# Kernel tuning notes

Measured on AMD Instinct MI355X. Metric: run time of the kernel, lower is better.

## Reference

```python
import jax, jax.numpy as jnp
import numpy as np

FH, FW = 38, 50          # stride-16 feature map of a 608x800 image
N_ROIS = 512
SCALE = 1.0 / 16.0
R = 7                    # roi_size -> 7x7 position-sensitive bins, 2x2 crop per bin
OUT_DIM = 10


def _conv(x, w, b, pad):
    # NCHW conv, stride 1, asymmetric 'same' padding for (k,1)/(1,k) kernels
    y = jax.lax.conv_general_dilated(
        x, w, (1, 1), [(pad[0], pad[0]), (pad[1], pad[1])],
        dimension_numbers=('NCHW', 'OIHW', 'NCHW'))
    return y + b[None, :, None, None]


def setup_inputs() -> dict:
    key = jax.random.key(0)
    ks = jax.random.split(key, 20)
    x = jax.random.normal(ks[0], (1, 2048, FH, FW), jnp.float32)
    # rois: unnormalized [x1,y1,x2,y2] in image coordinates, strictly inside the image
    img_h, img_w = FH * 16.0, FW * 16.0
    u = jax.random.uniform(ks[1], (N_ROIS, 4))
    x1 = u[:, 0] * (img_w * 0.5)
    y1 = u[:, 1] * (img_h * 0.5)
    x2 = x1 + 16.0 + u[:, 2] * (img_w - 17.0 - x1)
    y2 = y1 + 16.0 + u[:, 3] * (img_h - 17.0 - y1)
    rois = jnp.stack([x1, y1, x2, y2], axis=1)
    std = 0.01  # normal_init(0, 0.01)
    p = lambda k, shape: jax.random.normal(k, shape, jnp.float32) * std
    inp = {
        'x': x, 'rois': rois,
        'w_col_max': p(ks[2], (256, 2048, 15, 1)), 'b_col_max': jnp.zeros((256,), jnp.float32),
        'w_col':     p(ks[3], (490, 256, 1, 15)),  'b_col':     jnp.zeros((490,), jnp.float32),
        'w_row_max': p(ks[4], (256, 2048, 1, 15)), 'b_row_max': jnp.zeros((256,), jnp.float32),
        'w_row':     p(ks[5], (490, 256, 15, 1)),  'b_row':     jnp.zeros((490,), jnp.float32),
        'w_fc1':   p(ks[6], (2048, 490)), 'b_fc1':   jnp.zeros((2048,), jnp.float32),
        'w_score': p(ks[7], (81, 2048)),  'b_score': jnp.zeros((81,), jnp.float32),
        'w_loc':   p(ks[8], (324, 2048)), 'b_loc':   jnp.zeros((324,), jnp.float32),
    }
    return inp


def reference(x, rois, w_col_max, b_col_max, w_col, b_col,
              w_row_max, b_row_max, w_row, b_row,
              w_fc1, b_fc1, w_score, b_score, w_loc, b_loc):
    # ---- GlobalContextModule: large separable 15-tap convs ----
    h_col = _conv(_conv(x, w_col_max, b_col_max, (7, 0)), w_col, b_col, (0, 7))
    h_row = _conv(_conv(x, w_row_max, b_row_max, (0, 7)), w_row, b_row, (7, 0))
    h = jax.nn.relu(h_col + h_row)  # [1, 490, H, W]
    H, W = h.shape[2], h.shape[3]

    # ---- position-sensitive crop-and-resize + per-bin max, fully vectorized ----
    b = rois * SCALE / jnp.array([W, H, W, H], jnp.float32)  # normalized [x1,y1,x2,y2]
    xmin, ymin, xmax, ymax = b[:, 0], b[:, 1], b[:, 2], b[:, 3]
    step_x = (xmax - xmin) / R
    step_y = (ymax - ymin) / R
    # sample offsets: bin index (0..R-1) + crop sample (0 or 1); crop size 2 => samples at bin edges
    g = jnp.arange(R, dtype=jnp.float32)[None, :, None] + jnp.arange(2, dtype=jnp.float32)[None, None, :]
    ys = (ymin[:, None, None] + g * step_y[:, None, None]) * (H - 1)  # [N, R, 2]
    xs = (xmin[:, None, None] + g * step_x[:, None, None]) * (W - 1)  # [N, R, 2]

    def idx_w(v, vmax):
        v0 = jnp.floor(v)
        f = v - v0
        i0 = jnp.clip(v0, 0, vmax - 1).astype(jnp.int32)
        i1 = jnp.clip(v0 + 1.0, 0, vmax - 1).astype(jnp.int32)
        return i0, i1, f

    yi0, yi1, wy = idx_w(ys, H)
    xi0, xi1, wx = idx_w(xs, W)

    feat = h[0].reshape(R * R, OUT_DIM, H, W).transpose(0, 2, 3, 1)  # [49, H, W, 10]
    bidx = (jnp.arange(R)[:, None] * R + jnp.arange(R)[None, :])[None, :, :, None, None]  # [1,R,R,1,1]
    Y0 = yi0[:, :, None, :, None]; Y1 = yi1[:, :, None, :, None]  # [N,R,1,2,1]
    X0 = xi0[:, None, :, None, :]; X1 = xi1[:, None, :, None, :]  # [N,1,R,1,2]
    WY = wy[:, :, None, :, None, None]
    WX = wx[:, None, :, None, :, None]

    v00 = feat[bidx, Y0, X0]; v01 = feat[bidx, Y0, X1]
    v10 = feat[bidx, Y1, X0]; v11 = feat[bidx, Y1, X1]  # [N,R,R,2,2,10]
    top = v00 + (v01 - v00) * WX
    bot = v10 + (v11 - v10) * WX
    val = top + (bot - top) * WY
    pooled = val.max(axis=(3, 4))                       # [N, R, R, 10]
    flat = pooled.reshape(pooled.shape[0], -1)          # [N, 490], order = bin*10 + c

    fc1 = jax.nn.relu(flat @ w_fc1.T + b_fc1)           # [N, 2048]
    roi_cls_locs = fc1 @ w_loc.T + b_loc                # [N, 324]
    roi_scores = fc1 @ w_score.T + b_score              # [N, 81]
    return roi_cls_locs, roi_scores
```

## Files before the change

kernel.cpp:

```cpp
#include <hip/hip_runtime.h>
#include <math.h>

#define FW 50
#define FH 38
#define NPIX 1900
#define NROIS 512

#define CSH 2470
#define CSV 2650

typedef __bf16 bf16x8 __attribute__((ext_vector_type(8)));
typedef float  f32x4  __attribute__((ext_vector_type(4)));

__device__ __forceinline__ unsigned short f2b(float f) {
    unsigned int u = __float_as_uint(f);
    unsigned int r = (u + 0x7fffu + ((u >> 16) & 1u)) >> 16;
    return (unsigned short)r;
}


__global__ __launch_bounds__(256) void zero_us(unsigned short* __restrict__ p, int n) {
    int i = (blockIdx.x * 256 + threadIdx.x) * 8;
    if (i < n) { uint4 z; z.x = z.y = z.z = z.w = 0u; *(uint4*)(p + i) = z; }
}

__global__ __launch_bounds__(256) void cvt_bf16(
    const float* __restrict__ in, unsigned short* __restrict__ out, int n)
{
    int i = (blockIdx.x * 256 + threadIdx.x) * 4;
    if (i >= n) return;
    float4 v = *(const float4*)(in + i);
    ushort2 a, b;
    a.x = f2b(v.x); a.y = f2b(v.y);
    b.x = f2b(v.z); b.y = f2b(v.w);
    *(ushort2*)(out + i)     = a;
    *(ushort2*)(out + i + 2) = b;
}

__global__ __launch_bounds__(256) void cvt_pad(
    const float* __restrict__ in, unsigned short* __restrict__ out,
    int rows, int Kin, int Kout)
{
    int idx = blockIdx.x * 256 + threadIdx.x;
    if (idx >= rows * Kout) return;
    int rw = idx / Kout, k = idx - rw * Kout;
    out[idx] = (k < Kin) ? f2b(in[(size_t)rw * Kin + k]) : (unsigned short)0;
}

__global__ __launch_bounds__(256) void repack_w(
    const float* __restrict__ w, unsigned short* __restrict__ out, int n)
{
    int idx = blockIdx.x * 256 + threadIdx.x;
    if (idx >= n) return;
    int t = idx & 15;
    int oc = idx >> 4;
    out[idx] = (t < 15) ? f2b(w[oc * 15 + t]) : (unsigned short)0;
}

__global__ __launch_bounds__(256) void xpad_h(
    const float* __restrict__ xs, unsigned short* __restrict__ out)
{
    int idx = blockIdx.x * 256 + threadIdx.x;
    if (idx >= 2048 * CSH) return;
    int c = idx / CSH;
    int rem = idx - c * CSH;
    int y = rem / 65;
    int xc = rem - y * 65 - 7;
    unsigned short v = 0;
    if (xc >= 0 && xc < FW) v = f2b(xs[(c * FH + y) * FW + xc]);
    out[idx] = v;
}

__global__ __launch_bounds__(256) void xpad_v(
    const float* __restrict__ xs, unsigned short* __restrict__ out)
{
    int idx = blockIdx.x * 256 + threadIdx.x;
    if (idx >= 2048 * CSV) return;
    int c = idx / CSV;
    int rem = idx - c * CSV;
    int xx = rem / 53;
    int yc = rem - xx * 53 - 7;
    unsigned short v = 0;
    if (yc >= 0 && yc < FH) v = f2b(xs[(c * FH + yc) * FW + xx]);
    out[idx] = v;
}

__global__ __launch_bounds__(256) void conv_tap(
    const unsigned short* __restrict__ Wt,
    const unsigned short* __restrict__ Xp,
    float* __restrict__ P,
    int M, int Kp, int Mpad, int CS, int yMul, int xMul,
    int zMask, int zBits, int yMask, int xShift)
{
    const int id = blockIdx.x;
    const int zt = id & zMask;
    const int yt = (id >> zBits) & yMask;
    const int xt = id >> xShift;
    const int nsplit = zMask + 1;

    const int Ks = Kp / nsplit;
    const int k0 = zt * Ks;
    const int tid  = threadIdx.x;
    const int lane = tid & 63;
    const int wave = tid >> 6;
    const int mbase = yt * 128;
    const int pbase = xt * 64;

    __shared__ unsigned short As[128][40];
    __shared__ unsigned short Bt[64][40];

    const int a_row = tid >> 1;
    const int a_k16 = (tid & 1) << 4;
    const int a_src = min(mbase + a_row, M - 1);
    const unsigned short* Abase = Wt + (size_t)a_src * Kp + a_k16;

    const int b_pix = tid >> 2;
    const int q     = tid & 3;
    int p = pbase + b_pix;
    if (p > NPIX - 1) p = NPIX - 1;
    const int py = p / FW, px = p - py * FW;
    const int pixBase = py * yMul + px * xMul;
    const int eoff = pixBase + ((q & 1) << 3);
    const unsigned* __restrict__ Bdw = (const unsigned*)Xp;

    f32x4 acc[4][2];
#pragma unroll
    for (int i = 0; i < 4; ++i)
#pragma unroll
        for (int j = 0; j < 2; ++j)
#pragma unroll
            for (int r = 0; r < 4; ++r) acc[i][j][r] = 0.f;

    const int wy = (wave >> 1) * 64;
    const int wx = (wave & 1) * 32;
    const int lm = lane & 15;
    const int l8 = (lane >> 4) * 8;

    uint4 aR0, aR1;
    unsigned d[5];

    auto loadA = [&](int kt) {
        aR0 = *(const uint4*)(Abase + kt);
        aR1 = *(const uint4*)(Abase + kt + 8);
    };
    auto loadB = [&](int kt) {
        const int cg = (kt >> 4) + (q >> 1);
        const unsigned base = ((unsigned)(cg * CS + eoff)) >> 1;
#pragma unroll
        for (int j = 0; j < 5; ++j) d[j] = Bdw[base + j];
    };

    loadA(k0); loadB(k0);
    const unsigned sh = ((unsigned)(pixBase & 1)) << 4;

    for (int kt = k0; kt < k0 + Ks; kt += 32) {
        unsigned ob[4];
#pragma unroll
        for (int j = 0; j < 4; ++j)
            ob[j] = __builtin_amdgcn_alignbit(d[j + 1], d[j], sh);
        *(uint4*)&As[a_row][a_k16]     = aR0;
        *(uint4*)&As[a_row][a_k16 + 8] = aR1;
        *(uint4*)&Bt[b_pix][q << 3] = *(uint4*)&ob[0];
        __syncthreads();

        if (kt + 32 < k0 + Ks) { loadA(kt + 32); loadB(kt + 32); }

        bf16x8 af[4], bfr[2];
#pragma unroll
        for (int i = 0; i < 4; ++i)
            af[i]  = __builtin_bit_cast(bf16x8, *(const uint4*)&As[wy + i * 16 + lm][l8]);
#pragma unroll
        for (int j = 0; j < 2; ++j)
            bfr[j] = __builtin_bit_cast(bf16x8, *(const uint4*)&Bt[wx + j * 16 + lm][l8]);

#pragma unroll
        for (int i = 0; i < 4; ++i)
#pragma unroll
            for (int j = 0; j < 2; ++j)
                acc[i][j] = __builtin_amdgcn_mfma_f32_16x16x32_bf16(af[i], bfr[j], acc[i][j], 0, 0, 0);
        __syncthreads();
    }

    float* Pp = P + (size_t)zt * Mpad * NPIX;
#pragma unroll
    for (int i = 0; i < 4; ++i) {
        const int m0 = mbase + wy + i * 16 + (lane >> 4) * 4;
#pragma unroll
        for (int j = 0; j < 2; ++j) {
            const int pp = pbase + wx + j * 16 + lm;
            if (pp < NPIX) {
#pragma unroll
                for (int r = 0; r < 4; ++r)
                    Pp[(size_t)(m0 + r) * NPIX + pp] = acc[i][j][r];
            }
        }
    }
}

__global__ void reduce_pad(
    const float* __restrict__ P, int Mpad, int nsplit,
    const float* __restrict__ bias, int M,
    unsigned short* __restrict__ outb, int CS, int yMul, int xMul)
{
    int idx = blockIdx.x * 256 + threadIdx.x;
    if (idx >= M * NPIX) return;
    int o = idx / NPIX;
    int p = idx - o * NPIX;
    float s = bias[o];
    for (int sp = 0; sp < nsplit; ++sp)
        s += P[((size_t)sp * Mpad + o) * NPIX + p];
    int y = p / FW, x = p - y * FW;
    outb[(size_t)o * CS + y * yMul + x * xMul + 7] = f2b(s);
}

__global__ void reduce_bias(
    const float* __restrict__ P, int Mpad, int nsplit,
    const float* __restrict__ bias, int M,
    const float* __restrict__ addbuf, int relu,
    float* __restrict__ outf)
{
    int idx = blockIdx.x * blockDim.x + threadIdx.x;
    if (idx >= M * NPIX) return;
    int o = idx / NPIX;
    int p = idx - o * NPIX;
    float s = bias[o];
    for (int sp = 0; sp < nsplit; ++sp)
        s += P[((size_t)sp * Mpad + o) * NPIX + p];
    if (addbuf) s += addbuf[idx];
    if (relu) s = fmaxf(s, 0.f);
    outf[idx] = s;
}

__global__ __launch_bounds__(512) void pool_kernel(
    const float* __restrict__ h, const float* __restrict__ rois,
    unsigned short* __restrict__ pooledb)
{
    int n = blockIdx.x;
    int k = threadIdx.x;
    if (k >= 490) {
        pooledb[(size_t)n * 512 + k] = 0;
        return;
    }
    float x1 = rois[n * 4 + 0], y1 = rois[n * 4 + 1];
    float x2 = rois[n * 4 + 2], y2 = rois[n * 4 + 3];
    float xmin = x1 * (1.f / 16.f) / 50.f;
    float ymin = y1 * (1.f / 16.f) / 38.f;
    float xmax = x2 * (1.f / 16.f) / 50.f;
    float ymax = y2 * (1.f / 16.f) / 38.f;
    float step_x = (xmax - xmin) / 7.f;
    float step_y = (ymax - ymin) / 7.f;
    int bin = k / 10;
    int bi = bin / 7, bj = bin - bi * 7;
    const float* ch = h + (size_t)k * NPIX;
    float m = -INFINITY;
#pragma unroll
    for (int sy = 0; sy < 2; ++sy) {
        float yv = (ymin + (float)(bi + sy) * step_y) * 37.f;
        float y0 = floorf(yv);
        float fy = yv - y0;
        int yi0 = min(max((int)y0, 0), 37);
        int yi1 = min(max((int)y0 + 1, 0), 37);
#pragma unroll
        for (int sx = 0; sx < 2; ++sx) {
            float xv = (xmin + (float)(bj + sx) * step_x) * 49.f;
            float x0 = floorf(xv);
            float fx = xv - x0;
            int xi0 = min(max((int)x0, 0), 49);
            int xi1 = min(max((int)x0 + 1, 0), 49);
            float v00 = ch[yi0 * FW + xi0], v01 = ch[yi0 * FW + xi1];
            float v10 = ch[yi1 * FW + xi0], v11 = ch[yi1 * FW + xi1];
            float top = v00 + (v01 - v00) * fx;
            float bot = v10 + (v11 - v10) * fx;
            float val = top + (bot - top) * fy;
            m = fmaxf(m, val);
        }
    }
    pooledb[(size_t)n * 512 + k] = f2b(m);
}

__global__ __launch_bounds__(256) void fc_mfma(
    const unsigned short* __restrict__ Wb,
    const unsigned short* __restrict__ Act,
    float* __restrict__ P, int M, int Kld, int Mpad)
{
    const int Ks = Kld / gridDim.z;
    const int k0 = blockIdx.z * Ks;
    const int tid  = threadIdx.x;
    const int lane = tid & 63;
    const int wave = tid >> 6;
    const int mbase = blockIdx.x * 64;
    const int nbase = blockIdx.y * 64;

    __shared__ unsigned short As[64][40];
    __shared__ unsigned short Bs[64][40];

    const int s_r  = tid >> 2;
    const int s_k8 = (tid & 3) << 3;
    const int a_row = mbase + s_r;
    const bool a_ok = a_row < M;
    const unsigned short* Abase = Wb + (size_t)a_row * Kld + s_k8;
    const unsigned short* Bbase = Act + (size_t)(nbase + s_r) * Kld + s_k8;

    f32x4 acc[2][2];
#pragma unroll
    for (int i = 0; i < 2; ++i)
#pragma unroll
        for (int j = 0; j < 2; ++j)
#pragma unroll
            for (int r = 0; r < 4; ++r) acc[i][j][r] = 0.f;

    const int mh = (wave >> 1) * 32;
    const int nh = (wave & 1) * 32;
    const int lm = lane & 15;
    const int l8 = (lane >> 4) * 8;

    uint4 aReg, bReg;
    if (a_ok) aReg = *(const uint4*)(Abase + k0);
    else { aReg.x = aReg.y = aReg.z = aReg.w = 0u; }
    bReg = *(const uint4*)(Bbase + k0);

    for (int kt = k0; kt < k0 + Ks; kt += 32) {
        *(uint4*)&As[s_r][s_k8] = aReg;
        *(uint4*)&Bs[s_r][s_k8] = bReg;
        __syncthreads();

        if (kt + 32 < k0 + Ks) {
            if (a_ok) aReg = *(const uint4*)(Abase + kt + 32);
            bReg = *(const uint4*)(Bbase + kt + 32);
        }

        bf16x8 a0 = __builtin_bit_cast(bf16x8, *(const uint4*)&As[mh + lm][l8]);
        bf16x8 a1 = __builtin_bit_cast(bf16x8, *(const uint4*)&As[mh + 16 + lm][l8]);
        bf16x8 b0 = __builtin_bit_cast(bf16x8, *(const uint4*)&Bs[nh + lm][l8]);
        bf16x8 b1 = __builtin_bit_cast(bf16x8, *(const uint4*)&Bs[nh + 16 + lm][l8]);

        acc[0][0] = __builtin_amdgcn_mfma_f32_16x16x32_bf16(a0, b0, acc[0][0], 0, 0, 0);
        acc[0][1] = __builtin_amdgcn_mfma_f32_16x16x32_bf16(a0, b1, acc[0][1], 0, 0, 0);
        acc[1][0] = __builtin_amdgcn_mfma_f32_16x16x32_bf16(a1, b0, acc[1][0], 0, 0, 0);
        acc[1][1] = __builtin_amdgcn_mfma_f32_16x16x32_bf16(a1, b1, acc[1][1], 0, 0, 0);
        __syncthreads();
    }

#pragma unroll
    for (int ms = 0; ms < 2; ++ms)
#pragma unroll
        for (int ns = 0; ns < 2; ++ns) {
            int n  = nbase + nh + ns * 16 + lm;
            int m0 = mbase + mh + ms * 16 + (lane >> 4) * 4;
            float* Pp = P + ((size_t)blockIdx.z * NROIS + n) * Mpad + m0;
            *(f32x4*)Pp = acc[ms][ns];
        }
}

__global__ void fc_reduce(
    const float* __restrict__ P, int Mpad, int M, int nsplit,
    const float* __restrict__ bias, int relu,
    float* __restrict__ outf, unsigned short* __restrict__ outb)
{
    int idx = blockIdx.x * 256 + threadIdx.x;
    if (idx >= NROIS * M) return;
    int n = idx / M, m = idx - n * M;
    float s = bias[m];
    for (int sp = 0; sp < nsplit; ++sp)
        s += P[((size_t)sp * NROIS + n) * Mpad + m];
    if (relu) s = fmaxf(s, 0.f);
    if (outf) outf[idx] = s;
    if (outb) outb[idx] = f2b(s);
}

extern "C" void kernel_launch(void* const* d_in, const int* in_sizes, int n_in,
                              void* d_out, int out_size, void* d_ws, size_t ws_size,
                              hipStream_t stream) {
    const float* x         = (const float*)d_in[0];
    const float* rois      = (const float*)d_in[1];
    const float* w_col_max = (const float*)d_in[2];
    const float* b_col_max = (const float*)d_in[3];
    const float* w_col     = (const float*)d_in[4];
    const float* b_col     = (const float*)d_in[5];
    const float* w_row_max = (const float*)d_in[6];
    const float* b_row_max = (const float*)d_in[7];
    const float* w_row     = (const float*)d_in[8];
    const float* b_row     = (const float*)d_in[9];
    const float* w_fc1     = (const float*)d_in[10];
    const float* b_fc1     = (const float*)d_in[11];
    const float* w_score   = (const float*)d_in[12];
    const float* b_score   = (const float*)d_in[13];
    const float* w_loc     = (const float*)d_in[14];
    const float* b_loc     = (const float*)d_in[15];

    float* part = (float*)d_ws;
    unsigned short* XvU   = (unsigned short*)(part + 7782400);
    unsigned short* XhU   = XvU + 5427264;
    unsigned short* wbig  = XhU + 5058624;
    unsigned short* wc16  = wbig + 8388608;
    unsigned short* wr16  = wc16 + 2007040;
    unsigned short* c1colb= wr16 + 2007040;
    unsigned short* c1rowb= c1colb + 632384;
    unsigned short* wfc1b = c1rowb + 678464;
    unsigned short* pooledb = wfc1b + 1048576;
    unsigned short* fc1b  = pooledb + 262144;
    unsigned short* wlocb = fc1b + 1048576;
    unsigned short* wscoreb = wlocb + 663552;
    float* hcol = (float*)XvU;
    float* h    = (float*)XhU;

    xpad_v<<<21200, 256, 0, stream>>>(x, XvU);
    xpad_h<<<19760, 256, 0, stream>>>(x, XhU);
    zero_us<<<309, 256, 0, stream>>>(c1colb, 632384);
    zero_us<<<332, 256, 0, stream>>>(c1rowb, 678464);
    repack_w<<<32768, 256, 0, stream>>>(w_col_max, wbig, 8388608);
    repack_w<<<7840, 256, 0, stream>>>(w_col, wc16, 2007040);
    repack_w<<<7840, 256, 0, stream>>>(w_row, wr16, 2007040);
    cvt_pad <<<4096, 256, 0, stream>>>(w_fc1, wfc1b, 2048, 490, 512);
    cvt_bf16<<<648,  256, 0, stream>>>(w_loc, wlocb, 663552);
    cvt_bf16<<<162,  256, 0, stream>>>(w_score, wscoreb, 165888);

    conv_tap<<<960, 256, 0, stream>>>(wbig, XvU, part, 256, 32768, 256, CSV, 1, 53, 15, 4, 1, 5);
    reduce_pad<<<1900, 256, 0, stream>>>(part, 256, 16, b_col_max, 256, c1colb, CSH, 65, 1);
    repack_w<<<32768, 256, 0, stream>>>(w_row_max, wbig, 8388608);
    conv_tap<<<960, 256, 0, stream>>>(wbig, XhU, part, 256, 32768, 256, CSH, 65, 1, 15, 4, 1, 5);
    reduce_pad<<<1900, 256, 0, stream>>>(part, 256, 16, b_row_max, 256, c1rowb, CSV, 1, 53);

    conv_tap<<<960, 256, 0, stream>>>(wc16, c1colb, part, 490, 4096, 512, CSH, 65, 1, 7, 3, 3, 5);
    reduce_bias<<<3637, 256, 0, stream>>>(part, 512, 8, b_col, 490, nullptr, 0, hcol);
    conv_tap<<<960, 256, 0, stream>>>(wr16, c1rowb, part, 490, 4096, 512, CSV, 1, 53, 7, 3, 3, 5);
    reduce_bias<<<3637, 256, 0, stream>>>(part, 512, 8, b_row, 490, hcol, 1, h);

    pool_kernel<<<512, 512, 0, stream>>>(h, rois, pooledb);

    float* out = (float*)d_out;
    fc_mfma<<<dim3(32, 8, 2), 256, 0, stream>>>(wfc1b, pooledb, part, 2048, 512, 2048);
    fc_reduce<<<4096, 256, 0, stream>>>(part, 2048, 2048, 2, b_fc1, 1, nullptr, fc1b);
    fc_mfma<<<dim3(6, 8, 4), 256, 0, stream>>>(wlocb, fc1b, part, 324, 2048, 384);
    fc_reduce<<<648, 256, 0, stream>>>(part, 384, 324, 4, b_loc, 0, out, nullptr);
    fc_mfma<<<dim3(2, 8, 8), 256, 0, stream>>>(wscoreb, fc1b, part, 81, 2048, 128);
    fc_reduce<<<162, 256, 0, stream>>>(part, 128, 81, 8, b_score, 0, out + 512 * 324, nullptr);
}
```

Measured before the change: 465.0 us.

## Enlarge conv GEMM tile to 128x128 with 32x32 MFMA and double-buffered LDS

The conv_tap GEMM now uses a 128-pixel tile instead of 64, with each wave computing a 64x64 sub-tile through 32x32x16 bf16 MFMAs, which halves the launched blocks. LDS is double-buffered, so the trailing barrier per k-step is removed and each iteration keeps a single sync. Each B-load thread now fetches 9 dwords, covering 16 channels per pixel. The aim is more reuse of A and B per LDS load and less synchronisation, at the cost of fewer blocks (480) for occupancy and more registers per thread. The two zeroing launches are merged into one.

```diff
diff --git a/kernel.cpp b/kernel.cpp
--- a/kernel.cpp
+++ b/kernel.cpp
@@ -11,6 +11,7 @@
 
 typedef __bf16 bf16x8 __attribute__((ext_vector_type(8)));
 typedef float  f32x4  __attribute__((ext_vector_type(4)));
+typedef float  f32x16 __attribute__((ext_vector_type(16)));
 
 __device__ __forceinline__ unsigned short f2b(float f) {
     unsigned int u = __float_as_uint(f);
@@ -104,94 +105,102 @@
     const int lane = tid & 63;
     const int wave = tid >> 6;
     const int mbase = yt * 128;
-    const int pbase = xt * 64;
-
-    __shared__ unsigned short As[128][40];
-    __shared__ unsigned short Bt[64][40];
+    const int pbase = xt * 128;
+
+    __shared__ unsigned short As[2][128][40];
+    __shared__ unsigned short Bt[2][128][40];
 
     const int a_row = tid >> 1;
     const int a_k16 = (tid & 1) << 4;
     const int a_src = min(mbase + a_row, M - 1);
     const unsigned short* Abase = Wt + (size_t)a_src * Kp + a_k16;
 
-    const int b_pix = tid >> 2;
-    const int q     = tid & 3;
+    const int b_pix = tid >> 1;
+    const int bh    = tid & 1;
     int p = pbase + b_pix;
     if (p > NPIX - 1) p = NPIX - 1;
     const int py = p / FW, px = p - py * FW;
     const int pixBase = py * yMul + px * xMul;
-    const int eoff = pixBase + ((q & 1) << 3);
     const unsigned* __restrict__ Bdw = (const unsigned*)Xp;
 
-    f32x4 acc[4][2];
-#pragma unroll
-    for (int i = 0; i < 4; ++i)
+    f32x16 acc[2][2];
+#pragma unroll
+    for (int i = 0; i < 2; ++i)
 #pragma unroll
         for (int j = 0; j < 2; ++j)
 #pragma unroll
-            for (int r = 0; r < 4; ++r) acc[i][j][r] = 0.f;
+            for (int r = 0; r < 16; ++r) acc[i][j][r] = 0.f;
 
     const int wy = (wave >> 1) * 64;
-    const int wx = (wave & 1) * 32;
-    const int lm = lane & 15;
-    const int l8 = (lane >> 4) * 8;
+    const int wx = (wave & 1) * 64;
+    const int l5 = lane & 31;
+    const int l8 = (lane >> 5) * 8;
 
     uint4 aR0, aR1;
-    unsigned d[5];
+    unsigned d[9];
 
     auto loadA = [&](int kt) {
         aR0 = *(const uint4*)(Abase + kt);
         aR1 = *(const uint4*)(Abase + kt + 8);
     };
     auto loadB = [&](int kt) {
-        const int cg = (kt >> 4) + (q >> 1);
-        const unsigned base = ((unsigned)(cg * CS + eoff)) >> 1;
-#pragma unroll
-        for (int j = 0; j < 5; ++j) d[j] = Bdw[base + j];
+        const int cg = (kt >> 4) + bh;
+        const unsigned base = ((unsigned)(cg * CS + pixBase)) >> 1;
+#pragma unroll
+        for (int j = 0; j < 9; ++j) d[j] = Bdw[base + j];
     };
 
     loadA(k0); loadB(k0);
     const unsigned sh = ((unsigned)(pixBase & 1)) << 4;
 
+    int buf = 0;
     for (int kt = k0; kt < k0 + Ks; kt += 32) {
-        unsigned ob[4];
-#pragma unroll
-        for (int j = 0; j < 4; ++j)
+        unsigned ob[8];
+#pragma unroll
+        for (int j = 0; j < 8; ++j)
             ob[j] = __builtin_amdgcn_alignbit(d[j + 1], d[j], sh);
-        *(uint4*)&As[a_row][a_k16]     = aR0;
-        *(uint4*)&As[a_row][a_k16 + 8] = aR1;
-        *(uint4*)&Bt[b_pix][q << 3] = *(uint4*)&ob[0];
+        *(uint4*)&As[buf][a_row][a_k16]     = aR0;
+        *(uint4*)&As[buf][a_row][a_k16 + 8] = aR1;
+        *(uint4*)&Bt[buf][b_pix][bh * 16]     = *(uint4*)&ob[0];
+        *(uint4*)&Bt[buf][b_pix][bh * 16 + 8] = *(uint4*)&ob[4];
         __syncthreads();
 
         if (kt + 32 < k0 + Ks) { loadA(kt + 32); loadB(kt + 32); }
 
-        bf16x8 af[4], bfr[2];
-#pragma unroll
-        for (int i = 0; i < 4; ++i)
-            af[i]  = __builtin_bit_cast(bf16x8, *(const uint4*)&As[wy + i * 16 + lm][l8]);
-#pragma unroll
-        for (int j = 0; j < 2; ++j)
-            bfr[j] = __builtin_bit_cast(bf16x8, *(const uint4*)&Bt[wx + j * 16 + lm][l8]);
-
-#pragma unroll
-        for (int i = 0; i < 4; ++i)
-#pragma unroll
-            for (int j = 0; j < 2; ++j)
-                acc[i][j] = __builtin_amdgcn_mfma_f32_16x16x32_bf16(af[i], bfr[j], acc[i][j], 0, 0, 0);
-        __syncthreads();
+        bf16x8 af[2][2], bfr[2][2];
+#pragma unroll
+        for (int i = 0; i < 2; ++i)
+#pragma unroll
+            for (int kk = 0; kk < 2; ++kk) {
+                af[i][kk]  = __builtin_bit_cast(bf16x8,
+                    *(const uint4*)&As[buf][wy + i * 32 + l5][kk * 16 + l8]);
+                bfr[i][kk] = __builtin_bit_cast(bf16x8,
+                    *(const uint4*)&Bt[buf][wx + i * 32 + l5][kk * 16 + l8]);
+            }
+#pragma unroll
+        for (int kk = 0; kk < 2; ++kk)
+#pragma unroll
+            for (int i = 0; i < 2; ++i)
+#pragma unroll
+                for (int j = 0; j < 2; ++j)
+                    acc[i][j] = __builtin_amdgcn_mfma_f32_32x32x16_bf16(
+                        af[i][kk], bfr[j][kk], acc[i][j], 0, 0, 0);
+        buf ^= 1;
     }
 
     float* Pp = P + (size_t)zt * Mpad * NPIX;
 #pragma unroll
-    for (int i = 0; i < 4; ++i) {
-        const int m0 = mbase + wy + i * 16 + (lane >> 4) * 4;
+    for (int i = 0; i < 2; ++i) {
+        const int mb = mbase + wy + i * 32 + (lane >> 5) * 4;
 #pragma unroll
         for (int j = 0; j < 2; ++j) {
-            const int pp = pbase + wx + j * 16 + lm;
+            const int pp = pbase + wx + j * 32 + l5;
             if (pp < NPIX) {
 #pragma unroll
-                for (int r = 0; r < 4; ++r)
-                    Pp[(size_t)(m0 + r) * NPIX + pp] = acc[i][j][r];
+                for (int r = 0; r < 16; ++r) {
+                    const int m = mb + (r & 3) + 8 * (r >> 2);
+                    Pp[(size_t)m * NPIX + pp] = acc[i][j][r];
+                }
             }
         }
     }
@@ -406,8 +415,7 @@
 
     xpad_v<<<21200, 256, 0, stream>>>(x, XvU);
     xpad_h<<<19760, 256, 0, stream>>>(x, XhU);
-    zero_us<<<309, 256, 0, stream>>>(c1colb, 632384);
-    zero_us<<<332, 256, 0, stream>>>(c1rowb, 678464);
+    zero_us<<<641, 256, 0, stream>>>(c1colb, 1310848);
     repack_w<<<32768, 256, 0, stream>>>(w_col_max, wbig, 8388608);
     repack_w<<<7840, 256, 0, stream>>>(w_col, wc16, 2007040);
     repack_w<<<7840, 256, 0, stream>>>(w_row, wr16, 2007040);
@@ -415,15 +423,15 @@
     cvt_bf16<<<648,  256, 0, stream>>>(w_loc, wlocb, 663552);
     cvt_bf16<<<162,  256, 0, stream>>>(w_score, wscoreb, 165888);
 
-    conv_tap<<<960, 256, 0, stream>>>(wbig, XvU, part, 256, 32768, 256, CSV, 1, 53, 15, 4, 1, 5);
+    conv_tap<<<480, 256, 0, stream>>>(wbig, XvU, part, 256, 32768, 256, CSV, 1, 53, 15, 4, 1, 5);
     reduce_pad<<<1900, 256, 0, stream>>>(part, 256, 16, b_col_max, 256, c1colb, CSH, 65, 1);
     repack_w<<<32768, 256, 0, stream>>>(w_row_max, wbig, 8388608);
-    conv_tap<<<960, 256, 0, stream>>>(wbig, XhU, part, 256, 32768, 256, CSH, 65, 1, 15, 4, 1, 5);
+    conv_tap<<<480, 256, 0, stream>>>(wbig, XhU, part, 256, 32768, 256, CSH, 65, 1, 15, 4, 1, 5);
     reduce_pad<<<1900, 256, 0, stream>>>(part, 256, 16, b_row_max, 256, c1rowb, CSV, 1, 53);
 
-    conv_tap<<<960, 256, 0, stream>>>(wc16, c1colb, part, 490, 4096, 512, CSH, 65, 1, 7, 3, 3, 5);
+    conv_tap<<<480, 256, 0, stream>>>(wc16, c1colb, part, 490, 4096, 512, CSH, 65, 1, 7, 3, 3, 5);
     reduce_bias<<<3637, 256, 0, stream>>>(part, 512, 8, b_col, 490, nullptr, 0, hcol);
-    conv_tap<<<960, 256, 0, stream>>>(wr16, c1rowb, part, 490, 4096, 512, CSV, 1, 53, 7, 3, 3, 5);
+    conv_tap<<<480, 256, 0, stream>>>(wr16, c1rowb, part, 490, 4096, 512, CSV, 1, 53, 7, 3, 3, 5);
     reduce_bias<<<3637, 256, 0, stream>>>(part, 512, 8, b_row, 490, hcol, 1, h);
 
     pool_kernel<<<512, 512, 0, stream>>>(h, rois, pooledb);
```

New measurement: 423.0 us. 9.0% less time.
